# Performance work log

Measured on AMD Instinct MI355X. Metric: run time of the kernel, lower is better.

Reference implementation:

```python
import jax, jax.numpy as jnp
import numpy as np

N, D = 8192, 1024
Q = 4096
DK = 512
DV = 256


def setup_inputs() -> dict:
    key = jax.random.key(0)
    k1, k2, k3, k4, k5, k6 = jax.random.split(key, 6)
    return {
        "search_x": jax.random.normal(k1, (N, D), dtype=jnp.float32),
        "search_y": jax.random.normal(k2, (N, DV), dtype=jnp.float32),
        "query_x": jax.random.normal(k3, (Q, D), dtype=jnp.float32),
        "mask": jax.random.randint(k4, (Q, N), 0, 2, dtype=jnp.int64),
        "Wk": jax.random.normal(k5, (D, DK), dtype=jnp.float32) / np.sqrt(D),
        "Wq": jax.random.normal(k6, (D, DK), dtype=jnp.float32) / np.sqrt(D),
    }


def reference(search_x, search_y, query_x, mask, Wk, Wq):
    # key/query modules: bias-free linear projections (n_keys == 1 after _ensure_key_shape)
    keys = search_x @ Wk            # [N, DK]
    qk = query_x @ Wq               # [Q, DK]
    scale = 1.0 / jnp.sqrt(jnp.asarray(DK, dtype=keys.dtype))
    logits = (qk @ keys.T) * scale  # [Q, N]  (== broadcast mul+sum in original)
    # masked softmax over the search dimension (dim=1)
    m = mask > 0                    # [Q, N]
    neg = jnp.finfo(logits.dtype).min
    p = jax.nn.softmax(jnp.where(m, logits, neg), axis=1)
    p = jnp.where(m, p, 0.0)
    # values = noop_value_module(search_x, search_y) = search_y  [N, DV]
    res = p @ search_y              # [Q, DV]
    return res[:, None, :]          # [Q, n_keys=1, DV], matching original output shape
```

## Files before the change

kernel.cpp:

```cpp
#include <hip/hip_runtime.h>
#include <hip/hip_fp16.h>

typedef _Float16 half4v __attribute__((ext_vector_type(4)));
typedef _Float16 half8v __attribute__((ext_vector_type(8)));
typedef float floatx4 __attribute__((ext_vector_type(4)));

#define GLOBAL_AS __attribute__((address_space(1)))
#define LDS_AS __attribute__((address_space(3)))

__device__ __forceinline__ void async_copy16(const _Float16* g, _Float16* l) {
    __builtin_amdgcn_global_load_lds((const GLOBAL_AS unsigned int*)g,
                                     (LDS_AS unsigned int*)l, 16, 0, 0);
}

__global__ __launch_bounds__(256) void k_f32_to_f16_2(const float* __restrict__ a,
                                                      _Float16* __restrict__ oa, int na,
                                                      const float* __restrict__ b,
                                                      _Float16* __restrict__ ob, int nb) {
    int i = (blockIdx.x * 256 + threadIdx.x) * 4;
    const float* src;
    _Float16* dst;
    if (i < na) {
        src = a + i; dst = oa + i;
    } else {
        int j = i - na;
        if (j >= nb) return;
        src = b + j; dst = ob + j;
    }
    float4 v = *(const float4*)src;
    half4v h;
    h[0] = (_Float16)v.x; h[1] = (_Float16)v.y; h[2] = (_Float16)v.z; h[3] = (_Float16)v.w;
    *(half4v*)dst = h;
}

__global__ __launch_bounds__(256) void k_transpose_f16(const float* __restrict__ in,
                                                       _Float16* __restrict__ out,
                                                       int R, int C) {
    __shared__ float tile[32][33];
    int bc = blockIdx.x * 32;
    int br = blockIdx.y * 32;
    int tx = threadIdx.x & 31, ty = threadIdx.x >> 5;
#pragma unroll
    for (int i = 0; i < 32; i += 8)
        tile[ty + i][tx] = in[(size_t)(br + ty + i) * C + bc + tx];
    __syncthreads();
#pragma unroll
    for (int i = 0; i < 32; i += 8)
        out[(size_t)(bc + ty + i) * R + br + tx] = (_Float16)tile[tx][ty + i];
}

template <int OUT_MODE>
__global__ __launch_bounds__(256) void k_gemm_nt(const _Float16* __restrict__ A,
                                                 const _Float16* __restrict__ B,
                                                 void* __restrict__ C,
                                                 const int* __restrict__ Mask,
                                                 int M, int N, int K, int kChunk,
                                                 float scale) {
    __shared__ __align__(16) _Float16 As[128 * 64];
    __shared__ __align__(16) _Float16 Bs[128 * 64];
    const int tid  = threadIdx.x;
    const int lane = tid & 63;
    const int wave = tid >> 6;
    const int wm   = (wave >> 1) * 64;
    const int wn   = (wave & 1) * 64;
    const int quad = lane >> 4;
    const int lr   = lane & 15;
    const long m0 = (long)blockIdx.y * 128;
    const long n0 = (long)blockIdx.x * 128;
    const int kBegin = blockIdx.z * kChunk;
    const int kEnd   = kBegin + kChunk;

    floatx4 acc[4][4] = {};

    const int rl = lane >> 3;
    const int gc = (lane & 7) ^ rl;
    const long arow = m0 + wave * 32 + rl;
    const long brow = n0 + wave * 32 + rl;

    for (int kt = kBegin; kt < kEnd; kt += 64) {
        const _Float16* Ap = A + arow * (long)K + kt + gc * 8;
        const _Float16* Bp = B + brow * (long)K + kt + gc * 8;
        _Float16* Al = &As[(wave * 32) * 64];
        _Float16* Bl = &Bs[(wave * 32) * 64];
#pragma unroll
        for (int i = 0; i < 4; ++i) {
            async_copy16(Ap + (long)(i * 8) * K, Al + i * 8 * 64);
            async_copy16(Bp + (long)(i * 8) * K, Bl + i * 8 * 64);
        }
        __syncthreads();

#pragma unroll
        for (int kk = 0; kk < 64; kk += 32) {
            half8v af[4], bf[4];
            const int cg = (kk >> 3) + quad;
            const int sl = (cg ^ (lr & 7)) * 8;
#pragma unroll
            for (int i = 0; i < 4; ++i)
                af[i] = *(const half8v*)&As[(wm + i * 16 + lr) * 64 + sl];
#pragma unroll
            for (int j = 0; j < 4; ++j)
                bf[j] = *(const half8v*)&Bs[(wn + j * 16 + lr) * 64 + sl];
#pragma unroll
            for (int i = 0; i < 4; ++i)
#pragma unroll
                for (int j = 0; j < 4; ++j)
                    acc[i][j] = __builtin_amdgcn_mfma_f32_16x16x32_f16(af[i], bf[j], acc[i][j], 0, 0, 0);
        }
        __syncthreads();
    }

#pragma unroll
    for (int i = 0; i < 4; ++i) {
        long rbase = m0 + wm + i * 16 + quad * 4;
#pragma unroll
        for (int j = 0; j < 4; ++j) {
            long col = n0 + wn + j * 16 + lr;
#pragma unroll
            for (int r = 0; r < 4; ++r) {
                float val = acc[i][j][r] * scale;
                if (OUT_MODE == 0) {
                    ((_Float16*)C)[(rbase + r) * (long)N + col] = (_Float16)val;
                } else if (OUT_MODE == 1) {
                    ((float*)C)[(size_t)blockIdx.z * M * N + (rbase + r) * (long)N + col] = val;
                } else {
                    int mv = Mask[(rbase + r) * (long)N + col];
                    ((_Float16*)C)[(rbase + r) * (long)N + col] =
                        mv > 0 ? (_Float16)val : (_Float16)(-__builtin_inff());
                }
            }
        }
    }
}

template <int Z>
__global__ __launch_bounds__(256) void k_reduce(const float* __restrict__ part,
                                                float* __restrict__ out, int n) {
    int i = (blockIdx.x * 256 + threadIdx.x) * 4;
    if (i >= n) return;
    float4 s = *(const float4*)(part + i);
#pragma unroll
    for (int z = 1; z < Z; ++z) {
        float4 v = *(const float4*)(part + (size_t)z * n + i);
        s.x += v.x; s.y += v.y; s.z += v.z; s.w += v.w;
    }
    *(float4*)(out + i) = s;
}

__global__ __launch_bounds__(256) void k_softmax(_Float16* __restrict__ logits) {
    const int q   = blockIdx.x;
    const int tid = threadIdx.x;
    _Float16* row = logits + (size_t)q * 8192;

    float v[32];
    float lmax = -3.0e38f;
#pragma unroll
    for (int i = 0; i < 4; ++i) {
        int base = i * 2048 + tid * 8;
        half8v h = *(const half8v*)(row + base);
#pragma unroll
        for (int j = 0; j < 8; ++j) {
            v[i * 8 + j] = (float)h[j];
            lmax = fmaxf(lmax, v[i * 8 + j]);
        }
    }
#pragma unroll
    for (int off = 32; off > 0; off >>= 1) lmax = fmaxf(lmax, __shfl_xor(lmax, off, 64));
    __shared__ float redmax[4], redsum[4];
    if ((tid & 63) == 0) redmax[tid >> 6] = lmax;
    __syncthreads();
    lmax = fmaxf(fmaxf(redmax[0], redmax[1]), fmaxf(redmax[2], redmax[3]));

    float lsum = 0.f;
#pragma unroll
    for (int i = 0; i < 32; ++i) {
        float e = __expf(v[i] - lmax);
        v[i] = e;
        lsum += e;
    }
#pragma unroll
    for (int off = 32; off > 0; off >>= 1) lsum += __shfl_xor(lsum, off, 64);
    if ((tid & 63) == 0) redsum[tid >> 6] = lsum;
    __syncthreads();
    lsum = redsum[0] + redsum[1] + redsum[2] + redsum[3];
    float inv = lsum > 0.f ? 1.f / lsum : 0.f;

#pragma unroll
    for (int i = 0; i < 4; ++i) {
        int base = i * 2048 + tid * 8;
        half8v h;
#pragma unroll
        for (int j = 0; j < 8; ++j) h[j] = (_Float16)(v[i * 8 + j] * inv);
        *(half8v*)(row + base) = h;
    }
}

extern "C" void kernel_launch(void* const* d_in, const int* in_sizes, int n_in,
                              void* d_out, int out_size, void* d_ws, size_t ws_size,
                              hipStream_t stream) {
    const float* search_x = (const float*)d_in[0];
    const float* search_y = (const float*)d_in[1];
    const float* query_x  = (const float*)d_in[2];
    const int*   mask     = (const int*)d_in[3];
    const float* Wk       = (const float*)d_in[4];
    const float* Wq       = (const float*)d_in[5];
    (void)in_sizes; (void)n_in; (void)ws_size; (void)out_size;

    char* p = (char*)d_ws;
    _Float16* xh   = (_Float16*)p; p += (size_t)8192 * 1024 * 2;
    _Float16* qh   = (_Float16*)p; p += (size_t)4096 * 1024 * 2;
    _Float16* wkT  = (_Float16*)p; p += (size_t)512 * 1024 * 2;
    _Float16* wqT  = (_Float16*)p; p += (size_t)512 * 1024 * 2;
    _Float16* yT   = (_Float16*)p; p += (size_t)256 * 8192 * 2;
    _Float16* keys = (_Float16*)p; p += (size_t)8192 * 512 * 2;
    _Float16* qk   = (_Float16*)p; p += (size_t)4096 * 512 * 2;
    _Float16* lg   = (_Float16*)p; p += (size_t)4096 * 8192 * 2;
    float*    part = (float*)p;    p += (size_t)4 * 4096 * 256 * 4;

    k_f32_to_f16_2<<<12288, 256, 0, stream>>>(search_x, xh, 8192 * 1024,
                                              query_x, qh, 4096 * 1024);
    k_transpose_f16<<<dim3(16, 32), 256, 0, stream>>>(Wk, wkT, 1024, 512);
    k_transpose_f16<<<dim3(16, 32), 256, 0, stream>>>(Wq, wqT, 1024, 512);
    k_transpose_f16<<<dim3(8, 256), 256, 0, stream>>>(search_y, yT, 8192, 256);

    k_gemm_nt<0><<<dim3(4, 64, 1), 256, 0, stream>>>(xh, wkT, keys, nullptr,
                                                     8192, 512, 1024, 1024, 1.0f);
    k_gemm_nt<0><<<dim3(4, 32, 1), 256, 0, stream>>>(qh, wqT, qk, nullptr,
                                                     4096, 512, 1024, 1024, 1.0f);
    k_gemm_nt<2><<<dim3(64, 32, 1), 256, 0, stream>>>(qk, keys, lg, mask,
                                                      4096, 8192, 512, 512,
                                                      0.04419417382415922f);
    k_softmax<<<4096, 256, 0, stream>>>(lg);
    k_gemm_nt<1><<<dim3(2, 32, 4), 256, 0, stream>>>(lg, yT, part, nullptr,
                                                     4096, 256, 8192, 2048, 1.0f);
    k_reduce<4><<<1024, 256, 0, stream>>>(part, (float*)d_out, 4096 * 256);
}
```

Measured before the change: 393.6 us.

## Fuse logits, masked softmax and PV into split-K flash attention with bitmask

Replaces the materialized fp16 logits matrix, the separate softmax pass and the split-K PV GEMM with a flash-attention style kernel that computes QK^T tiles, applies an online masked softmax and accumulates P·V in registers. The search dimension is split into 8 chunks, and a combine kernel merges the partial results using their row max and sum. The int mask is first packed into a bitmask so the fused kernel reads 1 bit per element instead of 4 bytes, and the softmax scale is folded into the query projection. The aim is to remove the 64MB logits round trips and the mask traffic. The cost is a lower-occupancy fused kernel with many barriers, V fragments loaded straight from global memory, and a combine pass over 8 partial outputs.

```diff
diff --git a/kernel.cpp b/kernel.cpp
--- a/kernel.cpp
+++ b/kernel.cpp
@@ -49,13 +49,33 @@
         out[(size_t)(bc + ty + i) * R + br + tx] = (_Float16)tile[tx][ty + i];
 }
 
-template <int OUT_MODE>
+__global__ __launch_bounds__(256) void k_pack_mask(const int* __restrict__ mask,
+                                                   unsigned* __restrict__ mb) {
+    __shared__ unsigned nib[256];
+    const int* row = mask + (size_t)blockIdx.x * 8192;
+    unsigned* orow = mb + (size_t)blockIdx.x * 256;
+    const int tid = threadIdx.x;
+#pragma unroll
+    for (int pass = 0; pass < 8; ++pass) {
+        int4 v = *(const int4*)(row + pass * 1024 + tid * 4);
+        unsigned nb = (unsigned)(v.x > 0) | ((unsigned)(v.y > 0) << 1) |
+                      ((unsigned)(v.z > 0) << 2) | ((unsigned)(v.w > 0) << 3);
+        nib[tid] = nb;
+        __syncthreads();
+        if (tid < 32) {
+            unsigned w = 0;
+#pragma unroll
+            for (int t = 0; t < 8; ++t) w |= nib[tid * 8 + t] << (t * 4);
+            orow[pass * 32 + tid] = w;
+        }
+        __syncthreads();
+    }
+}
+
 __global__ __launch_bounds__(256) void k_gemm_nt(const _Float16* __restrict__ A,
                                                  const _Float16* __restrict__ B,
-                                                 void* __restrict__ C,
-                                                 const int* __restrict__ Mask,
-                                                 int M, int N, int K, int kChunk,
-                                                 float scale) {
+                                                 _Float16* __restrict__ C,
+                                                 int M, int N, int K, float scale) {
     __shared__ __align__(16) _Float16 As[128 * 64];
     __shared__ __align__(16) _Float16 Bs[128 * 64];
     const int tid  = threadIdx.x;
@@ -67,8 +87,6 @@
     const int lr   = lane & 15;
     const long m0 = (long)blockIdx.y * 128;
     const long n0 = (long)blockIdx.x * 128;
-    const int kBegin = blockIdx.z * kChunk;
-    const int kEnd   = kBegin + kChunk;
 
     floatx4 acc[4][4] = {};
 
@@ -77,7 +95,7 @@
     const long arow = m0 + wave * 32 + rl;
     const long brow = n0 + wave * 32 + rl;
 
-    for (int kt = kBegin; kt < kEnd; kt += 64) {
+    for (int kt = 0; kt < K; kt += 64) {
         const _Float16* Ap = A + arow * (long)K + kt + gc * 8;
         const _Float16* Bp = B + brow * (long)K + kt + gc * 8;
         _Float16* Al = &As[(wave * 32) * 64];
@@ -116,82 +134,235 @@
         for (int j = 0; j < 4; ++j) {
             long col = n0 + wn + j * 16 + lr;
 #pragma unroll
+            for (int r = 0; r < 4; ++r)
+                C[(rbase + r) * (long)N + col] = (_Float16)(acc[i][j][r] * scale);
+        }
+    }
+}
+
+__global__ __launch_bounds__(512) void k_flash(const _Float16* __restrict__ Qk,
+                                               const _Float16* __restrict__ Keys,
+                                               const _Float16* __restrict__ Vt,
+                                               const unsigned* __restrict__ Mb,
+                                               float* __restrict__ Opart,
+                                               float* __restrict__ Mpart,
+                                               float* __restrict__ Lpart) {
+    __shared__ __align__(16) _Float16 As[128 * 64];
+    __shared__ __align__(16) _Float16 Bs[128 * 64];
+    __shared__ __align__(16) _Float16 Ps[2][128 * 64];
+    __shared__ float redbuf[8][64];
+
+    const int tid  = threadIdx.x;
+    const int lane = tid & 63;
+    const int wave = tid >> 6;
+    const int quad = lane >> 4;
+    const int lr   = lane & 15;
+    const int wm2  = (wave >> 2) * 64;
+    const int wn2  = (wave & 3) * 32;
+    const int dvo  = (wave & 3) * 64;
+    const int wg4  = (wave >> 2) * 4;
+    const long q0  = (long)blockIdx.x * 128;
+    const long n0beg = (long)blockIdx.y * 1024;
+
+    floatx4 o[4][4] = {};
+    float m_[4][4], l_[4][4];
+#pragma unroll
+    for (int i = 0; i < 4; ++i)
+#pragma unroll
+        for (int r = 0; r < 4; ++r) { m_[i][r] = -1.0e30f; l_[i][r] = 0.f; }
+
+    const int rl = lane >> 3;
+    const int gc = (lane & 7) ^ rl;
+    const long arow = q0 + wave * 16 + rl;
+
+    for (int nt = 0; nt < 8; ++nt) {
+        const long n0 = n0beg + nt * 128;
+        floatx4 s[4][2] = {};
+        for (int kt = 0; kt < 512; kt += 64) {
+            const _Float16* Ap = Qk + arow * 512 + kt + gc * 8;
+            const _Float16* Bp = Keys + (n0 + wave * 16 + rl) * 512 + kt + gc * 8;
+            _Float16* Al = &As[(wave * 16) * 64];
+            _Float16* Bl = &Bs[(wave * 16) * 64];
+#pragma unroll
+            for (int i = 0; i < 2; ++i) {
+                async_copy16(Ap + (long)(i * 8) * 512, Al + i * 8 * 64);
+                async_copy16(Bp + (long)(i * 8) * 512, Bl + i * 8 * 64);
+            }
+            __syncthreads();
+#pragma unroll
+            for (int kk = 0; kk < 64; kk += 32) {
+                const int cg = (kk >> 3) + quad;
+                const int sl = (cg ^ (lr & 7)) * 8;
+                half8v af[4], bf[2];
+#pragma unroll
+                for (int i = 0; i < 4; ++i)
+                    af[i] = *(const half8v*)&As[(wm2 + i * 16 + lr) * 64 + sl];
+#pragma unroll
+                for (int j = 0; j < 2; ++j)
+                    bf[j] = *(const half8v*)&Bs[(wn2 + j * 16 + lr) * 64 + sl];
+#pragma unroll
+                for (int i = 0; i < 4; ++i)
+#pragma unroll
+                    for (int j = 0; j < 2; ++j)
+                        s[i][j] = __builtin_amdgcn_mfma_f32_16x16x32_f16(af[i], bf[j], s[i][j], 0, 0, 0);
+            }
+            __syncthreads();
+        }
+
+        float sv[4][2][4];
+        unsigned wbit[4][4];
+        float tmax[4][4];
+#pragma unroll
+        for (int i = 0; i < 4; ++i)
+#pragma unroll
             for (int r = 0; r < 4; ++r) {
-                float val = acc[i][j][r] * scale;
-                if (OUT_MODE == 0) {
-                    ((_Float16*)C)[(rbase + r) * (long)N + col] = (_Float16)val;
-                } else if (OUT_MODE == 1) {
-                    ((float*)C)[(size_t)blockIdx.z * M * N + (rbase + r) * (long)N + col] = val;
-                } else {
-                    int mv = Mask[(rbase + r) * (long)N + col];
-                    ((_Float16*)C)[(rbase + r) * (long)N + col] =
-                        mv > 0 ? (_Float16)val : (_Float16)(-__builtin_inff());
+                const int tl = wm2 + i * 16 + quad * 4 + r;
+                const unsigned w = Mb[(size_t)(q0 + tl) * 256 + (size_t)((n0 + wn2) >> 5)];
+                wbit[i][r] = w;
+                float tm = -1.0e30f;
+#pragma unroll
+                for (int j = 0; j < 2; ++j) {
+                    const unsigned b = (w >> (j * 16 + lr)) & 1u;
+                    const float val = b ? s[i][j][r] : -1.0e30f;
+                    sv[i][j][r] = val;
+                    tm = fmaxf(tm, val);
                 }
-            }
-        }
-    }
-}
-
-template <int Z>
-__global__ __launch_bounds__(256) void k_reduce(const float* __restrict__ part,
-                                                float* __restrict__ out, int n) {
-    int i = (blockIdx.x * 256 + threadIdx.x) * 4;
-    if (i >= n) return;
-    float4 s = *(const float4*)(part + i);
-#pragma unroll
-    for (int z = 1; z < Z; ++z) {
-        float4 v = *(const float4*)(part + (size_t)z * n + i);
-        s.x += v.x; s.y += v.y; s.z += v.z; s.w += v.w;
-    }
-    *(float4*)(out + i) = s;
-}
-
-__global__ __launch_bounds__(256) void k_softmax(_Float16* __restrict__ logits) {
-    const int q   = blockIdx.x;
-    const int tid = threadIdx.x;
-    _Float16* row = logits + (size_t)q * 8192;
-
-    float v[32];
-    float lmax = -3.0e38f;
-#pragma unroll
-    for (int i = 0; i < 4; ++i) {
-        int base = i * 2048 + tid * 8;
-        half8v h = *(const half8v*)(row + base);
-#pragma unroll
-        for (int j = 0; j < 8; ++j) {
-            v[i * 8 + j] = (float)h[j];
-            lmax = fmaxf(lmax, v[i * 8 + j]);
-        }
-    }
-#pragma unroll
-    for (int off = 32; off > 0; off >>= 1) lmax = fmaxf(lmax, __shfl_xor(lmax, off, 64));
-    __shared__ float redmax[4], redsum[4];
-    if ((tid & 63) == 0) redmax[tid >> 6] = lmax;
-    __syncthreads();
-    lmax = fmaxf(fmaxf(redmax[0], redmax[1]), fmaxf(redmax[2], redmax[3]));
-
-    float lsum = 0.f;
-#pragma unroll
-    for (int i = 0; i < 32; ++i) {
-        float e = __expf(v[i] - lmax);
-        v[i] = e;
-        lsum += e;
-    }
-#pragma unroll
-    for (int off = 32; off > 0; off >>= 1) lsum += __shfl_xor(lsum, off, 64);
-    if ((tid & 63) == 0) redsum[tid >> 6] = lsum;
-    __syncthreads();
-    lsum = redsum[0] + redsum[1] + redsum[2] + redsum[3];
-    float inv = lsum > 0.f ? 1.f / lsum : 0.f;
-
-#pragma unroll
-    for (int i = 0; i < 4; ++i) {
-        int base = i * 2048 + tid * 8;
-        half8v h;
-#pragma unroll
-        for (int j = 0; j < 8; ++j) h[j] = (_Float16)(v[i * 8 + j] * inv);
-        *(half8v*)(row + base) = h;
-    }
+#pragma unroll
+                for (int off = 1; off < 16; off <<= 1)
+                    tm = fmaxf(tm, __shfl_xor(tm, off, 64));
+                tmax[i][r] = tm;
+            }
+        if (lr == 0) {
+#pragma unroll
+            for (int i = 0; i < 4; ++i)
+#pragma unroll
+                for (int r = 0; r < 4; ++r)
+                    redbuf[wave][i * 16 + quad * 4 + r] = tmax[i][r];
+        }
+        __syncthreads();
+#pragma unroll
+        for (int i = 0; i < 4; ++i)
+#pragma unroll
+            for (int r = 0; r < 4; ++r) {
+                const int rr = i * 16 + quad * 4 + r;
+                float t = fmaxf(fmaxf(redbuf[wg4][rr], redbuf[wg4 + 1][rr]),
+                                fmaxf(redbuf[wg4 + 2][rr], redbuf[wg4 + 3][rr]));
+                const float mn = fmaxf(m_[i][r], t);
+                const float f  = __expf(m_[i][r] - mn);
+                m_[i][r] = mn;
+                l_[i][r] *= f;
+#pragma unroll
+                for (int jv = 0; jv < 4; ++jv) o[i][jv][r] *= f;
+            }
+        __syncthreads();
+
+        const int ktile = wn2 >> 6;
+        float psum[4][4];
+#pragma unroll
+        for (int i = 0; i < 4; ++i)
+#pragma unroll
+            for (int r = 0; r < 4; ++r) {
+                const int tl = wm2 + i * 16 + quad * 4 + r;
+                const unsigned w = wbit[i][r];
+                float ps = 0.f;
+#pragma unroll
+                for (int j = 0; j < 2; ++j) {
+                    const unsigned b = (w >> (j * 16 + lr)) & 1u;
+                    const float e = b ? __expf(sv[i][j][r] - m_[i][r]) : 0.f;
+                    const int col  = wn2 + j * 16 + lr;
+                    const int slot = (((col & 63) >> 3) ^ (tl & 7));
+                    Ps[ktile][tl * 64 + slot * 8 + (col & 7)] = (_Float16)e;
+                    ps += e;
+                }
+#pragma unroll
+                for (int off = 1; off < 16; off <<= 1) ps += __shfl_xor(ps, off, 64);
+                psum[i][r] = ps;
+            }
+        if (lr == 0) {
+#pragma unroll
+            for (int i = 0; i < 4; ++i)
+#pragma unroll
+                for (int r = 0; r < 4; ++r)
+                    redbuf[wave][i * 16 + quad * 4 + r] = psum[i][r];
+        }
+        __syncthreads();
+#pragma unroll
+        for (int i = 0; i < 4; ++i)
+#pragma unroll
+            for (int r = 0; r < 4; ++r) {
+                const int rr = i * 16 + quad * 4 + r;
+                l_[i][r] += redbuf[wg4][rr] + redbuf[wg4 + 1][rr] +
+                            redbuf[wg4 + 2][rr] + redbuf[wg4 + 3][rr];
+            }
+
+#pragma unroll
+        for (int kp = 0; kp < 2; ++kp) {
+#pragma unroll
+            for (int kk = 0; kk < 64; kk += 32) {
+                const int cg = (kk >> 3) + quad;
+                const int sl = (cg ^ (lr & 7)) * 8;
+                half8v af[4], bf[4];
+#pragma unroll
+                for (int i = 0; i < 4; ++i)
+                    af[i] = *(const half8v*)&Ps[kp][(wm2 + i * 16 + lr) * 64 + sl];
+#pragma unroll
+                for (int j = 0; j < 4; ++j)
+                    bf[j] = *(const half8v*)(Vt + (size_t)(dvo + j * 16 + lr) * 8192 +
+                                             n0 + kp * 64 + kk + quad * 8);
+#pragma unroll
+                for (int i = 0; i < 4; ++i)
+#pragma unroll
+                    for (int j = 0; j < 4; ++j)
+                        o[i][j] = __builtin_amdgcn_mfma_f32_16x16x32_f16(af[i], bf[j], o[i][j], 0, 0, 0);
+            }
+        }
+    }
+
+    const size_t obase = (size_t)blockIdx.y * 4096 + (size_t)q0;
+#pragma unroll
+    for (int i = 0; i < 4; ++i)
+#pragma unroll
+        for (int r = 0; r < 4; ++r) {
+            const int row = wm2 + i * 16 + quad * 4 + r;
+#pragma unroll
+            for (int j = 0; j < 4; ++j) {
+                const int col = dvo + j * 16 + lr;
+                Opart[(obase + row) * 256 + col] = o[i][j][r];
+            }
+        }
+    if (lr == 0 && (wave & 3) == 0) {
+#pragma unroll
+        for (int i = 0; i < 4; ++i)
+#pragma unroll
+            for (int r = 0; r < 4; ++r) {
+                const int row = wm2 + i * 16 + quad * 4 + r;
+                Mpart[obase + row] = m_[i][r];
+                Lpart[obase + row] = l_[i][r];
+            }
+    }
+}
+
+__global__ __launch_bounds__(256) void k_combine(const float* __restrict__ Opart,
+                                                 const float* __restrict__ Mpart,
+                                                 const float* __restrict__ Lpart,
+                                                 float* __restrict__ out) {
+    const int q  = blockIdx.x;
+    const int dv = threadIdx.x;
+    float ms[8];
+    float M = -1.0e30f;
+#pragma unroll
+    for (int s = 0; s < 8; ++s) {
+        ms[s] = Mpart[s * 4096 + q];
+        M = fmaxf(M, ms[s]);
+    }
+    float L = 0.f, acc = 0.f;
+#pragma unroll
+    for (int s = 0; s < 8; ++s) {
+        const float w = __expf(ms[s] - M);
+        L += Lpart[s * 4096 + q] * w;
+        acc += Opart[((size_t)s * 4096 + q) * 256 + dv] * w;
+    }
+    out[(size_t)q * 256 + dv] = (L > 0.f) ? acc / L : 0.f;
 }
 
 extern "C" void kernel_launch(void* const* d_in, const int* in_sizes, int n_in,
@@ -206,31 +377,28 @@
     (void)in_sizes; (void)n_in; (void)ws_size; (void)out_size;
 
     char* p = (char*)d_ws;
-    _Float16* xh   = (_Float16*)p; p += (size_t)8192 * 1024 * 2;
-    _Float16* qh   = (_Float16*)p; p += (size_t)4096 * 1024 * 2;
-    _Float16* wkT  = (_Float16*)p; p += (size_t)512 * 1024 * 2;
-    _Float16* wqT  = (_Float16*)p; p += (size_t)512 * 1024 * 2;
-    _Float16* yT   = (_Float16*)p; p += (size_t)256 * 8192 * 2;
-    _Float16* keys = (_Float16*)p; p += (size_t)8192 * 512 * 2;
-    _Float16* qk   = (_Float16*)p; p += (size_t)4096 * 512 * 2;
-    _Float16* lg   = (_Float16*)p; p += (size_t)4096 * 8192 * 2;
-    float*    part = (float*)p;    p += (size_t)4 * 4096 * 256 * 4;
+    _Float16* xh    = (_Float16*)p; p += (size_t)8192 * 1024 * 2;
+    _Float16* qh    = (_Float16*)p; p += (size_t)4096 * 1024 * 2;
+    _Float16* wkT   = (_Float16*)p; p += (size_t)512 * 1024 * 2;
+    _Float16* wqT   = (_Float16*)p; p += (size_t)512 * 1024 * 2;
+    _Float16* yT    = (_Float16*)p; p += (size_t)256 * 8192 * 2;
+    _Float16* keys  = (_Float16*)p; p += (size_t)8192 * 512 * 2;
+    _Float16* qk    = (_Float16*)p; p += (size_t)4096 * 512 * 2;
+    unsigned* mbits = (unsigned*)p; p += (size_t)4096 * 256 * 4;
+    float*    Opart = (float*)p;    p += (size_t)8 * 4096 * 256 * 4;
+    float*    Mpart = (float*)p;    p += (size_t)8 * 4096 * 4;
+    float*    Lpart = (float*)p;    p += (size_t)8 * 4096 * 4;
 
     k_f32_to_f16_2<<<12288, 256, 0, stream>>>(search_x, xh, 8192 * 1024,
                                               query_x, qh, 4096 * 1024);
     k_transpose_f16<<<dim3(16, 32), 256, 0, stream>>>(Wk, wkT, 1024, 512);
     k_transpose_f16<<<dim3(16, 32), 256, 0, stream>>>(Wq, wqT, 1024, 512);
     k_transpose_f16<<<dim3(8, 256), 256, 0, stream>>>(search_y, yT, 8192, 256);
-
-    k_gemm_nt<0><<<dim3(4, 64, 1), 256, 0, stream>>>(xh, wkT, keys, nullptr,
-                                                     8192, 512, 1024, 1024, 1.0f);
-    k_gemm_nt<0><<<dim3(4, 32, 1), 256, 0, stream>>>(qh, wqT, qk, nullptr,
-                                                     4096, 512, 1024, 1024, 1.0f);
-    k_gemm_nt<2><<<dim3(64, 32, 1), 256, 0, stream>>>(qk, keys, lg, mask,
-                                                      4096, 8192, 512, 512,
-                                                      0.04419417382415922f);
-    k_softmax<<<4096, 256, 0, stream>>>(lg);
-    k_gemm_nt<1><<<dim3(2, 32, 4), 256, 0, stream>>>(lg, yT, part, nullptr,
-                                                     4096, 256, 8192, 2048, 1.0f);
-    k_reduce<4><<<1024, 256, 0, stream>>>(part, (float*)d_out, 4096 * 256);
-}
+    k_pack_mask<<<4096, 256, 0, stream>>>(mask, mbits);
+
+    k_gemm_nt<<<dim3(4, 64), 256, 0, stream>>>(xh, wkT, keys, 8192, 512, 1024, 1.0f);
+    k_gemm_nt<<<dim3(4, 32), 256, 0, stream>>>(qh, wqT, qk, 4096, 512, 1024,
+                                               0.04419417382415922f);
+    k_flash<<<dim3(32, 8), 512, 0, stream>>>(qk, keys, yT, mbits, Opart, Mpart, Lpart);
+    k_combine<<<4096, 256, 0, stream>>>(Opart, Mpart, Lpart, (float*)d_out);
+}
```

New measurement: 479.7 us. 1.22x slower.
